# Optimization experiments

Measured on AMD Instinct MI355X. Metric: run time of the kernel, lower is better.

The kernel has to match this reference:

```python
import jax, jax.numpy as jnp
import numpy as np

DIM = 1024          # moe_cfg.dim
INTER = 1024        # moe_cfg.moe_inter_dim
E = 8               # moe_cfg.n_routed_experts
TOPK = 2            # moe_cfg.n_activated_experts
ROUTE_SCALE = 1.0
SHARED_INTER = 2048 # n_shared_experts * moe_inter_dim
B, S = 4, 2048


def setup_inputs() -> dict:
    key = jax.random.key(0)
    ks = jax.random.split(key, 10)
    def w(k, shape, scale=0.02):
        return jax.random.normal(k, shape, jnp.float32) * scale
    return {
        "x": jax.random.normal(ks[0], (B, S, DIM), jnp.float32),
        # Gate (nn.Linear(dim, n_routed_experts, bias=True))
        "gate_w": w(ks[1], (E, DIM)),
        "gate_b": jnp.zeros((E,), jnp.float32),
        # Routed experts, stacked on leading E axis (torch Linear convention: [out, in])
        "w1": w(ks[2], (E, INTER, DIM)), "b1": jnp.zeros((E, INTER), jnp.float32),
        "w3": w(ks[3], (E, INTER, DIM)), "b3": jnp.zeros((E, INTER), jnp.float32),
        "w2": w(ks[4], (E, DIM, INTER)), "b2": jnp.zeros((E, DIM), jnp.float32),
        # Shared expert MLP(dim, n_shared_experts * moe_inter_dim)
        "ws1": w(ks[5], (SHARED_INTER, DIM)), "bs1": jnp.zeros((SHARED_INTER,), jnp.float32),
        "ws3": w(ks[6], (SHARED_INTER, DIM)), "bs3": jnp.zeros((SHARED_INTER,), jnp.float32),
        "ws2": w(ks[7], (DIM, SHARED_INTER)), "bs2": jnp.zeros((DIM,), jnp.float32),
    }


def _moe_forward(x, gate_w, gate_b, w1, b1, w3, b3, w2, b2,
                 ws1, bs1, ws3, bs3, ws2, bs2):
    Bq, Sq, D = x.shape
    xt = x.reshape(-1, D)  # [T, D], T = B*S
    # ---- Gate: softmax scores in fp32, top-k routing (eval mode: no usage buffers) ----
    logits = (xt @ gate_w.T + gate_b).astype(jnp.float32)  # [T, E]
    scores = jax.nn.softmax(logits, axis=-1)
    top_w, top_i = jax.lax.top_k(scores, TOPK)             # values == gathered scores
    weights = (top_w * ROUTE_SCALE).astype(x.dtype)        # [T, topk]
    # Dense combine weights [T, E]: zero for unrouted experts (math identical to dispatch)
    gate_dense = jnp.sum(jax.nn.one_hot(top_i, E, dtype=x.dtype) * weights[..., None], axis=1)
    # ---- Routed experts: SwiGLU FFN per expert (dropout p=0 -> identity) ----
    def expert(w1e, b1e, w3e, b3e, w2e, b2e):
        h = jax.nn.silu(xt @ w1e.T + b1e) * (xt @ w3e.T + b3e)  # [T, INTER]
        return h @ w2e.T + b2e                                   # [T, D]
    outs = jax.vmap(expert)(w1, b1, w3, b3, w2, b2)  # [E, T, D]
    y = jnp.einsum('etd,te->td', outs, gate_dense)   # weighted combine
    # ---- Shared expert MLP (SwiGLU) ----
    z = (jax.nn.silu(xt @ ws1.T + bs1) * (xt @ ws3.T + bs3)) @ ws2.T + bs2
    return (y + z).reshape(Bq, Sq, D)


def reference(x, gate_w, gate_b, w1, b1, w3, b3, w2, b2,
              ws1, bs1, ws3, bs3, ws2, bs2):
    return _moe_forward(x, gate_w, gate_b, w1, b1, w3, b3, w2, b2,
                        ws1, bs1, ws3, bs3, ws2, bs2)
```

## Files before the change

kernel.cpp:

```cpp
#include <hip/hip_runtime.h>
#include <stdint.h>
#include <stddef.h>

#define T_TOK  8192
#define DIMK   1024
#define INTERK 1024
#define NEXP   8
#define SINT   2048
#define CAP    17408
#define RTMAX  136

typedef float  f32x4  __attribute__((ext_vector_type(4)));
typedef short  bf16x8 __attribute__((ext_vector_type(8)));

typedef __attribute__((address_space(1))) const unsigned int gas_u32;
typedef __attribute__((address_space(3))) unsigned int las_u32;

__device__ __forceinline__ void gload16(const void* g, void* l) {
  __builtin_amdgcn_global_load_lds((gas_u32*)g, (las_u32*)l, 16, 0, 0);
}

__device__ __forceinline__ unsigned short f2b(float f) {
  unsigned int u = __float_as_uint(f);
  u = (u + 0x7FFFu + ((u >> 16) & 1u)) >> 16;
  return (unsigned short)u;
}
__device__ __forceinline__ float b2f(unsigned short h) {
  return __uint_as_float(((unsigned int)h) << 16);
}

__global__ __launch_bounds__(256) void cvt_kernel(const float4* __restrict__ in,
                                                  unsigned short* __restrict__ out, int n4) {
  int i = blockIdx.x * 256 + threadIdx.x;
  if (i >= n4) return;
  float4 v = in[i];
  ushort4 o;
  o.x = f2b(v.x); o.y = f2b(v.y); o.z = f2b(v.z); o.w = f2b(v.w);
  *reinterpret_cast<ushort4*>(&out[(size_t)i * 4]) = o;
}

template <int ROWS_PER_E, int K4>
__global__ __launch_bounds__(256) void cvt_w13_kernel(
    const float4* __restrict__ w1, const float4* __restrict__ w3,
    unsigned short* __restrict__ out, int n ) {
  int idx = blockIdx.x * 256 + threadIdx.x;
  int is3 = idx >= n;
  int i = is3 ? idx - n : idx;
  if (i >= n) return;
  int r  = i / K4;
  int kc = i - r * K4;
  int e  = r / ROWS_PER_E;
  int rr = r - e * ROWS_PER_E;
  int g  = rr >> 4;
  size_t dst_r = (size_t)e * (2 * ROWS_PER_E) + g * 32 + (is3 ? 16 : 0) + (rr & 15);
  float4 v = (is3 ? w3 : w1)[i];
  ushort4 o;
  o.x = f2b(v.x); o.y = f2b(v.y); o.z = f2b(v.z); o.w = f2b(v.w);
  *reinterpret_cast<ushort4*>(&out[(dst_r * K4 + kc) * 4]) = o;
}

__global__ __launch_bounds__(256) void gate_kernel(
    const float* __restrict__ x, const float* __restrict__ gw, const float* __restrict__ gb,
    int* __restrict__ top_i, float* __restrict__ top_w) {
  int t    = blockIdx.x * 4 + (threadIdx.x >> 6);
  int lane = threadIdx.x & 63;
  const float* xr = x + (size_t)t * DIMK;
  float acc[NEXP];
#pragma unroll
  for (int e = 0; e < NEXP; ++e) acc[e] = 0.f;
  for (int i = lane; i < DIMK; i += 64) {
    float xv = xr[i];
#pragma unroll
    for (int e = 0; e < NEXP; ++e) acc[e] += xv * gw[e * DIMK + i];
  }
#pragma unroll
  for (int e = 0; e < NEXP; ++e) {
    float v = acc[e];
#pragma unroll
    for (int off = 32; off > 0; off >>= 1) v += __shfl_down(v, off, 64);
    acc[e] = v;
  }
  if (lane == 0) {
    float lg[NEXP];
#pragma unroll
    for (int e = 0; e < NEXP; ++e) lg[e] = acc[e] + gb[e];
    int i0 = 0;
#pragma unroll
    for (int e = 1; e < NEXP; ++e) if (lg[e] > lg[i0]) i0 = e;
    int i1 = (i0 == 0) ? 1 : 0;
#pragma unroll
    for (int e = 0; e < NEXP; ++e) if (e != i0 && lg[e] > lg[i1]) i1 = e;
    float mx = lg[i0], s = 0.f;
#pragma unroll
    for (int e = 0; e < NEXP; ++e) s += expf(lg[e] - mx);
    top_i[t * 2]     = i0;
    top_i[t * 2 + 1] = i1;
    top_w[t * 2]     = expf(lg[i0] - mx) / s;
    top_w[t * 2 + 1] = expf(lg[i1] - mx) / s;
  }
}

__global__ __launch_bounds__(512) void route_build_kernel(
    const int* __restrict__ top_i, int* __restrict__ order, int* __restrict__ pos,
    int* __restrict__ poff_g) {
  __shared__ int cnt[NEXP][512];
  __shared__ int base[NEXP][512];
  __shared__ int totals[NEXP];
  __shared__ int poff_s[NEXP + 1];
  int tid = threadIdx.x;
  int lane = tid & 63, w = tid >> 6;
  const int t0 = tid * 16;

  int c[NEXP];
#pragma unroll
  for (int e = 0; e < NEXP; ++e) c[e] = 0;
  for (int j = 0; j < 16; ++j) {
    int e0 = top_i[(t0 + j) * 2];
    int e1 = top_i[(t0 + j) * 2 + 1];
#pragma unroll
    for (int e = 0; e < NEXP; ++e) c[e] += (e0 == e) + (e1 == e);
  }
#pragma unroll
  for (int e = 0; e < NEXP; ++e) cnt[e][tid] = c[e];
  __syncthreads();

  {
    int running = 0;
    for (int ch = 0; ch < 8; ++ch) {
      int v = cnt[w][ch * 64 + lane];
      int incl = v;
#pragma unroll
      for (int off = 1; off < 64; off <<= 1) {
        int u = __shfl_up(incl, off, 64);
        if (lane >= off) incl += u;
      }
      base[w][ch * 64 + lane] = running + incl - v;
      running += __shfl(incl, 63, 64);
    }
    if (lane == 0) totals[w] = running;
  }
  __syncthreads();

  if (tid == 0) {
    int off = 0;
#pragma unroll
    for (int e = 0; e < NEXP; ++e) {
      poff_s[e] = off;
      off += (totals[e] + 127) & ~127;
    }
    poff_s[NEXP] = off;
#pragma unroll
    for (int e = 0; e <= NEXP; ++e) poff_g[e] = poff_s[e];
  }
  __syncthreads();

  int cur[NEXP];
#pragma unroll
  for (int e = 0; e < NEXP; ++e) cur[e] = poff_s[e] + base[e][tid];
  for (int j = 0; j < 16; ++j) {
    int t = t0 + j;
#pragma unroll
    for (int k = 0; k < 2; ++k) {
      int ei = top_i[t * 2 + k];
      int p = 0;
#pragma unroll
      for (int e = 0; e < NEXP; ++e)
        if (ei == e) { p = cur[e]; cur[e] = p + 1; }
      order[p]       = t;
      pos[t * 2 + k] = p;
    }
  }

#pragma unroll
  for (int e = 0; e < NEXP; ++e) {
    int s = poff_s[e] + totals[e], en = poff_s[e + 1];
    for (int i = s + tid; i < en; i += 512) order[i] = 0;
  }
}

template <bool EXPERTS, bool GATHER, int EPI>
__global__ __launch_bounds__(256) void gemm_kernel(
    const unsigned short* __restrict__ A, int lda,
    const int* __restrict__ order, const int* __restrict__ poff,
    const unsigned short* __restrict__ B,
    const float* __restrict__ bias1, const float* __restrict__ bias3,
    size_t wstride, int bstride, int K,
    void* __restrict__ outp, int ldo) {
  __shared__ unsigned short As[128 * 64];
  __shared__ unsigned short Bs[128 * 64];

  int rowbase = blockIdx.x * 128;
  int expert  = 0;
  if (EXPERTS) {
    if (rowbase >= poff[NEXP]) return;
    while (expert < NEXP - 1 && rowbase >= poff[expert + 1]) ++expert;
  }
  const unsigned short* Be = B + (size_t)expert * wstride;

  int tid = threadIdx.x;
  int lane = tid & 63, w = tid >> 6, wr = w >> 1, wc = w & 1;
  int ncolbase = blockIdx.y * 128;

  size_t arow[4], brow[4];
#pragma unroll
  for (int it = 0; it < 4; ++it) {
    int c = it * 256 + tid;
    int r = c >> 3;
    int sub = (c & 7) ^ (r & 7);
    int gr = GATHER ? order[rowbase + r] : (rowbase + r);
    arow[it] = (size_t)gr * lda + (size_t)(sub * 8);
    brow[it] = (size_t)(ncolbase + r) * K + (size_t)(sub * 8);
  }

  f32x4 acc[4][4];
#pragma unroll
  for (int m = 0; m < 4; ++m)
#pragma unroll
    for (int n = 0; n < 4; ++n) acc[m][n] = f32x4{0.f, 0.f, 0.f, 0.f};

  for (int kb = 0; kb < K; kb += 64) {
#pragma unroll
    for (int it = 0; it < 4; ++it) {
      int c = it * 256 + tid;
      gload16(A + arow[it] + kb, &As[(size_t)c * 8]);
      gload16(Be + brow[it] + kb, &Bs[(size_t)c * 8]);
    }
    __syncthreads();
#pragma unroll
    for (int kk = 0; kk < 2; ++kk) {
      bf16x8 a[4], b[4];
#pragma unroll
      for (int m = 0; m < 4; ++m) {
        int ra = wr * 64 + m * 16 + (lane & 15);
        int sa = (kk * 4 + (lane >> 4)) ^ (ra & 7);
        a[m] = *(const bf16x8*)&As[ra * 64 + sa * 8];
      }
#pragma unroll
      for (int n = 0; n < 4; ++n) {
        int rb = wc * 64 + n * 16 + (lane & 15);
        int sb = (kk * 4 + (lane >> 4)) ^ (rb & 7);
        b[n] = *(const bf16x8*)&Bs[rb * 64 + sb * 8];
      }
#pragma unroll
      for (int m = 0; m < 4; ++m)
#pragma unroll
        for (int n = 0; n < 4; ++n)
          acc[m][n] = __builtin_amdgcn_mfma_f32_16x16x32_bf16(a[m], b[n], acc[m][n], 0, 0, 0);
    }
    __syncthreads();
  }

  if (EPI == 0) {
#pragma unroll
    for (int m = 0; m < 4; ++m)
#pragma unroll
      for (int np = 0; np < 2; ++np) {
        int realcol = (ncolbase >> 1) + wc * 32 + np * 16 + (lane & 15);
        float bb1 = bias1[bstride * expert + realcol];
        float bb3 = bias3[bstride * expert + realcol];
#pragma unroll
        for (int j = 0; j < 4; ++j) {
          int row  = rowbase + wr * 64 + m * 16 + (lane >> 4) * 4 + j;
          float a1 = acc[m][2 * np][j] + bb1;
          float a3 = acc[m][2 * np + 1][j] + bb3;
          float hv = (a1 / (1.f + __expf(-a1))) * a3;
          ((unsigned short*)outp)[(size_t)row * ldo + realcol] = f2b(hv);
        }
      }
  } else {
#pragma unroll
    for (int m = 0; m < 4; ++m)
#pragma unroll
      for (int n = 0; n < 4; ++n) {
        int col  = ncolbase + wc * 64 + n * 16 + (lane & 15);
        float bb = bias1[bstride * expert + col];
#pragma unroll
        for (int j = 0; j < 4; ++j) {
          int row = rowbase + wr * 64 + m * 16 + (lane >> 4) * 4 + j;
          float v = acc[m][n][j] + bb;
          if (EPI == 2)
            ((float*)outp)[(size_t)row * ldo + col] = v;
          else
            ((unsigned short*)outp)[(size_t)row * ldo + col] = f2b(v);
        }
      }
  }
}

__global__ __launch_bounds__(256) void combine_kernel(
    float* __restrict__ out, const unsigned short* __restrict__ y,
    const int* __restrict__ pos, const float* __restrict__ tw) {
  size_t idx = (size_t)blockIdx.x * 256 + threadIdx.x;
  if (idx >= (size_t)T_TOK * DIMK) return;
  int t = (int)(idx >> 10);
  int d = (int)(idx & 1023);
  int p0 = pos[t * 2], p1 = pos[t * 2 + 1];
  float w0 = tw[t * 2], w1 = tw[t * 2 + 1];
  out[idx] += w0 * b2f(y[(size_t)p0 * DIMK + d]) + w1 * b2f(y[(size_t)p1 * DIMK + d]);
}

extern "C" void kernel_launch(void* const* d_in, const int* in_sizes, int n_in,
                              void* d_out, int out_size, void* d_ws, size_t ws_size,
                              hipStream_t stream) {
  const float* x   = (const float*)d_in[0];
  const float* gw  = (const float*)d_in[1];
  const float* gb  = (const float*)d_in[2];
  const float* w1  = (const float*)d_in[3];
  const float* b1  = (const float*)d_in[4];
  const float* w3  = (const float*)d_in[5];
  const float* b3  = (const float*)d_in[6];
  const float* w2  = (const float*)d_in[7];
  const float* b2  = (const float*)d_in[8];
  const float* ws1 = (const float*)d_in[9];
  const float* bs1 = (const float*)d_in[10];
  const float* ws3 = (const float*)d_in[11];
  const float* bs3 = (const float*)d_in[12];
  const float* ws2 = (const float*)d_in[13];
  const float* bs2 = (const float*)d_in[14];
  float* out = (float*)d_out;
  (void)in_sizes; (void)n_in; (void)out_size; (void)ws_size;

  char* p = (char*)d_ws;
  auto alloc = [&](size_t bytes) -> void* {
    void* r = (void*)p;
    p += (bytes + 255) & ~(size_t)255;
    return r;
  };
  unsigned short* xb    = (unsigned short*)alloc((size_t)T_TOK * DIMK * 2);
  unsigned short* w13r  = (unsigned short*)alloc((size_t)NEXP * 2 * INTERK * DIMK * 2);
  unsigned short* w2b   = (unsigned short*)alloc((size_t)NEXP * DIMK * INTERK * 2);
  unsigned short* w13s  = (unsigned short*)alloc((size_t)2 * SINT * DIMK * 2);
  unsigned short* ws2b  = (unsigned short*)alloc((size_t)DIMK * SINT * 2);
  unsigned short* h     = (unsigned short*)alloc((size_t)CAP * INTERK * 2);
  unsigned short* yb    = (unsigned short*)alloc((size_t)CAP * DIMK * 2);
  unsigned short* hs    = (unsigned short*)alloc((size_t)T_TOK * SINT * 2);
  int*   top_i  = (int*)alloc((size_t)T_TOK * 2 * 4);
  float* top_w  = (float*)alloc((size_t)T_TOK * 2 * 4);
  int*   pos    = (int*)alloc((size_t)T_TOK * 2 * 4);
  int*   order  = (int*)alloc((size_t)CAP * 4);
  int*   poff   = (int*)alloc(64);

  auto cvt = [&](const float* src, unsigned short* dst, size_t n) {
    int n4 = (int)(n / 4);
    cvt_kernel<<<(n4 + 255) / 256, 256, 0, stream>>>((const float4*)src, dst, n4);
  };
  cvt(x,   xb,   (size_t)T_TOK * DIMK);
  cvt(w2,  w2b,  (size_t)NEXP * DIMK * INTERK);
  cvt(ws2, ws2b, (size_t)DIMK * SINT);

  {
    int n = NEXP * INTERK * (DIMK / 4);
    cvt_w13_kernel<INTERK, DIMK / 4><<<(2 * n + 255) / 256, 256, 0, stream>>>(
        (const float4*)w1, (const float4*)w3, w13r, n);
  }
  {
    int n = SINT * (DIMK / 4);
    cvt_w13_kernel<SINT, DIMK / 4><<<(2 * n + 255) / 256, 256, 0, stream>>>(
        (const float4*)ws1, (const float4*)ws3, w13s, n);
  }

  gate_kernel<<<T_TOK / 4, 256, 0, stream>>>(x, gw, gb, top_i, top_w);
  route_build_kernel<<<1, 512, 0, stream>>>(top_i, order, pos, poff);

  gemm_kernel<true, true, 0><<<dim3(RTMAX, (2 * INTERK) / 128), 256, 0, stream>>>(
      xb, DIMK, order, poff, w13r, b1, b3,
      (size_t)2 * INTERK * DIMK, INTERK, DIMK, h, INTERK);
  gemm_kernel<true, false, 1><<<dim3(RTMAX, DIMK / 128), 256, 0, stream>>>(
      h, INTERK, (const int*)nullptr, poff, w2b, b2, (const float*)nullptr,
      (size_t)DIMK * INTERK, DIMK, INTERK, (void*)yb, DIMK);

  gemm_kernel<false, false, 0><<<dim3(T_TOK / 128, (2 * SINT) / 128), 256, 0, stream>>>(
      xb, DIMK, (const int*)nullptr, (const int*)nullptr, w13s, bs1, bs3,
      (size_t)0, 0, DIMK, hs, SINT);
  gemm_kernel<false, false, 2><<<dim3(T_TOK / 128, DIMK / 128), 256, 0, stream>>>(
      hs, SINT, (const int*)nullptr, (const int*)nullptr, ws2b, bs2, (const float*)nullptr,
      (size_t)0, 0, SINT, (void*)out, DIMK);

  combine_kernel<<<(T_TOK * DIMK) / 256, 256, 0, stream>>>(out, yb, pos, top_w);
}
```

Baseline: 421.9 us.

## Use 256-row GEMM tiles with double-buffered LDS and async global-to-LDS prefetch

Replaces the 128x128 GEMM with a 512-thread, 256x128-tile kernel that double-buffers A and B tiles in LDS. The next K-slice is prefetched with global_load_lds while the current one feeds MFMA, using explicit vmcnt waits, plain s_barrier and raised wave priority around the MFMA section. Expert padding is raised to multiples of 256 to match the taller tile, and capacity is enlarged. The aim is to hide global-load latency and reuse each B tile across more rows, at the cost of more padded rows per expert, higher LDS use and fewer blocks.

```diff
diff --git a/kernel.cpp b/kernel.cpp
--- a/kernel.cpp
+++ b/kernel.cpp
@@ -7,8 +7,8 @@
 #define INTERK 1024
 #define NEXP   8
 #define SINT   2048
-#define CAP    17408
-#define RTMAX  136
+#define CAP    18432
+#define RT256  72
 
 typedef float  f32x4  __attribute__((ext_vector_type(4)));
 typedef short  bf16x8 __attribute__((ext_vector_type(8)));
@@ -27,6 +27,12 @@
 }
 __device__ __forceinline__ float b2f(unsigned short h) {
   return __uint_as_float(((unsigned int)h) << 16);
+}
+
+__device__ __forceinline__ void barrier_nodrain() {
+  asm volatile("" ::: "memory");
+  __builtin_amdgcn_s_barrier();
+  asm volatile("" ::: "memory");
 }
 
 __global__ __launch_bounds__(256) void cvt_kernel(const float4* __restrict__ in,
@@ -146,7 +152,7 @@
 #pragma unroll
     for (int e = 0; e < NEXP; ++e) {
       poff_s[e] = off;
-      off += (totals[e] + 127) & ~127;
+      off += (totals[e] + 255) & ~255;
     }
     poff_s[NEXP] = off;
 #pragma unroll
@@ -178,18 +184,19 @@
   }
 }
 
+#define A_ELE  16384
+#define B_ELE  8192
 template <bool EXPERTS, bool GATHER, int EPI>
-__global__ __launch_bounds__(256) void gemm_kernel(
+__global__ __launch_bounds__(512) void gemm256_kernel(
     const unsigned short* __restrict__ A, int lda,
     const int* __restrict__ order, const int* __restrict__ poff,
     const unsigned short* __restrict__ B,
     const float* __restrict__ bias1, const float* __restrict__ bias3,
     size_t wstride, int bstride, int K,
     void* __restrict__ outp, int ldo) {
-  __shared__ unsigned short As[128 * 64];
-  __shared__ unsigned short Bs[128 * 64];
-
-  int rowbase = blockIdx.x * 128;
+  __shared__ unsigned short lds[2 * A_ELE + 2 * B_ELE];
+
+  int rowbase = blockIdx.x * 256;
   int expert  = 0;
   if (EXPERTS) {
     if (rowbase >= poff[NEXP]) return;
@@ -198,18 +205,25 @@
   const unsigned short* Be = B + (size_t)expert * wstride;
 
   int tid = threadIdx.x;
-  int lane = tid & 63, w = tid >> 6, wr = w >> 1, wc = w & 1;
+  int lane = tid & 63, wid = tid >> 6;
+  int wr = wid >> 1, wc = wid & 1;
   int ncolbase = blockIdx.y * 128;
 
-  size_t arow[4], brow[4];
-#pragma unroll
-  for (int it = 0; it < 4; ++it) {
-    int c = it * 256 + tid;
-    int r = c >> 3;
-    int sub = (c & 7) ^ (r & 7);
+  size_t aoff[4], boff[2];
+#pragma unroll
+  for (int l = 0; l < 4; ++l) {
+    int g = l * 512 + tid;
+    int r = g >> 3;
+    int sub = (g & 7) ^ (r & 7);
     int gr = GATHER ? order[rowbase + r] : (rowbase + r);
-    arow[it] = (size_t)gr * lda + (size_t)(sub * 8);
-    brow[it] = (size_t)(ncolbase + r) * K + (size_t)(sub * 8);
+    aoff[l] = (size_t)gr * lda + (size_t)(sub * 8);
+  }
+#pragma unroll
+  for (int l = 0; l < 2; ++l) {
+    int g = l * 512 + tid;
+    int r = g >> 3;
+    int sub = (g & 7) ^ (r & 7);
+    boff[l] = (size_t)(ncolbase + r) * K + (size_t)(sub * 8);
   }
 
   f32x4 acc[4][4];
@@ -218,14 +232,35 @@
 #pragma unroll
     for (int n = 0; n < 4; ++n) acc[m][n] = f32x4{0.f, 0.f, 0.f, 0.f};
 
-  for (int kb = 0; kb < K; kb += 64) {
-#pragma unroll
-    for (int it = 0; it < 4; ++it) {
-      int c = it * 256 + tid;
-      gload16(A + arow[it] + kb, &As[(size_t)c * 8]);
-      gload16(Be + brow[it] + kb, &Bs[(size_t)c * 8]);
+  const int NT = K >> 6;
+
+#pragma unroll
+  for (int l = 0; l < 4; ++l)
+    gload16(A + aoff[l], &lds[(size_t)(l * 512 + tid) * 8]);
+#pragma unroll
+  for (int l = 0; l < 2; ++l)
+    gload16(Be + boff[l], &lds[2 * A_ELE + (size_t)(l * 512 + tid) * 8]);
+
+  for (int t = 0; t < NT; ++t) {
+    int cur = t & 1;
+    if (t + 1 < NT) {
+      int kb = (t + 1) << 6;
+      int nxt = cur ^ 1;
+#pragma unroll
+      for (int l = 0; l < 4; ++l)
+        gload16(A + aoff[l] + kb, &lds[(size_t)nxt * A_ELE + (size_t)(l * 512 + tid) * 8]);
+#pragma unroll
+      for (int l = 0; l < 2; ++l)
+        gload16(Be + boff[l] + kb, &lds[2 * A_ELE + (size_t)nxt * B_ELE + (size_t)(l * 512 + tid) * 8]);
+      asm volatile("s_waitcnt vmcnt(6)" ::: "memory");
+    } else {
+      asm volatile("s_waitcnt vmcnt(0)" ::: "memory");
     }
-    __syncthreads();
+    barrier_nodrain();
+
+    const unsigned short* Ab = &lds[(size_t)cur * A_ELE];
+    const unsigned short* Bb = &lds[2 * A_ELE + (size_t)cur * B_ELE];
+    __builtin_amdgcn_s_setprio(1);
 #pragma unroll
     for (int kk = 0; kk < 2; ++kk) {
       bf16x8 a[4], b[4];
@@ -233,13 +268,13 @@
       for (int m = 0; m < 4; ++m) {
         int ra = wr * 64 + m * 16 + (lane & 15);
         int sa = (kk * 4 + (lane >> 4)) ^ (ra & 7);
-        a[m] = *(const bf16x8*)&As[ra * 64 + sa * 8];
+        a[m] = *(const bf16x8*)&Ab[ra * 64 + sa * 8];
       }
 #pragma unroll
       for (int n = 0; n < 4; ++n) {
         int rb = wc * 64 + n * 16 + (lane & 15);
         int sb = (kk * 4 + (lane >> 4)) ^ (rb & 7);
-        b[n] = *(const bf16x8*)&Bs[rb * 64 + sb * 8];
+        b[n] = *(const bf16x8*)&Bb[rb * 64 + sb * 8];
       }
 #pragma unroll
       for (int m = 0; m < 4; ++m)
@@ -247,7 +282,9 @@
         for (int n = 0; n < 4; ++n)
           acc[m][n] = __builtin_amdgcn_mfma_f32_16x16x32_bf16(a[m], b[n], acc[m][n], 0, 0, 0);
     }
-    __syncthreads();
+    __builtin_amdgcn_s_setprio(0);
+    asm volatile("s_waitcnt lgkmcnt(0)" ::: "memory");
+    barrier_nodrain();
   }
 
   if (EPI == 0) {
@@ -362,17 +399,17 @@
   gate_kernel<<<T_TOK / 4, 256, 0, stream>>>(x, gw, gb, top_i, top_w);
   route_build_kernel<<<1, 512, 0, stream>>>(top_i, order, pos, poff);
 
-  gemm_kernel<true, true, 0><<<dim3(RTMAX, (2 * INTERK) / 128), 256, 0, stream>>>(
+  gemm256_kernel<true, true, 0><<<dim3(RT256, (2 * INTERK) / 128), 512, 0, stream>>>(
       xb, DIMK, order, poff, w13r, b1, b3,
       (size_t)2 * INTERK * DIMK, INTERK, DIMK, h, INTERK);
-  gemm_kernel<true, false, 1><<<dim3(RTMAX, DIMK / 128), 256, 0, stream>>>(
+  gemm256_kernel<true, false, 1><<<dim3(RT256, DIMK / 128), 512, 0, stream>>>(
       h, INTERK, (const int*)nullptr, poff, w2b, b2, (const float*)nullptr,
       (size_t)DIMK * INTERK, DIMK, INTERK, (void*)yb, DIMK);
 
-  gemm_kernel<false, false, 0><<<dim3(T_TOK / 128, (2 * SINT) / 128), 256, 0, stream>>>(
+  gemm256_kernel<false, false, 0><<<dim3(T_TOK / 256, (2 * SINT) / 128), 512, 0, stream>>>(
       xb, DIMK, (const int*)nullptr, (const int*)nullptr, w13s, bs1, bs3,
       (size_t)0, 0, DIMK, hs, SINT);
-  gemm_kernel<false, false, 2><<<dim3(T_TOK / 128, DIMK / 128), 256, 0, stream>>>(
+  gemm256_kernel<false, false, 2><<<dim3(T_TOK / 256, DIMK / 128), 512, 0, stream>>>(
       hs, SINT, (const int*)nullptr, (const int*)nullptr, ws2b, bs2, (const float*)nullptr,
       (size_t)0, 0, SINT, (void*)out, DIMK);
 
```

New measurement: 398.6 us. 1.06x faster.
